# Kernel optimization log

Measured on AMD Instinct MI355X. Metric: run time of the kernel, lower is better.

## Reference

```python
import jax, jax.numpy as jnp
import numpy as np

B, N = 8192, 20
D_IN = 256       # input_dim / neigh_input_dim
G_IN = 128       # geto_dims_in
H = 201 * 3      # hidden_dim, model_size='small'
D_OUT = 256      # output_dim


def _glorot(key, shape):
    lim = np.sqrt(6.0 / (shape[0] + shape[1]))
    return jax.random.uniform(key, shape, jnp.float32, -lim, lim)


def setup_inputs() -> dict:
    key = jax.random.key(0)
    ks = jax.random.split(key, 16)
    return {
        "self_vecs": jax.random.normal(ks[0], (B, D_IN), jnp.float32),
        "neigh_vecs": jax.random.normal(ks[1], (B, N, D_IN), jnp.float32),
        "self_geto": jax.random.normal(ks[2], (B, G_IN), jnp.float32),
        "neigh_geto": jax.random.normal(ks[3], (B, N, G_IN), jnp.float32),
        # feat MLP (relu)
        "W_feat": _glorot(ks[4], (D_IN, H)),
        "b_feat": jnp.zeros((H,), jnp.float32),
        # geto MLP (relu)
        "W_geto": _glorot(ks[5], (G_IN, H)),
        "b_geto": jnp.zeros((H,), jnp.float32),
        # geto-concat MLP (softmax act)
        "W_concat": _glorot(ks[6], (G_IN, H)),
        "b_concat": jnp.zeros((H,), jnp.float32),
        # combine weights
        "self_feat_w": _glorot(ks[7], (D_IN, D_OUT)),
        "self_geto_w": _glorot(ks[8], (G_IN, D_OUT)),
        "combined_geto": _glorot(ks[9], (H, 2 * D_OUT)),
        "neigh_feat_w": _glorot(ks[10], (H, D_OUT)),
        "neigh_geto_w": _glorot(ks[11], (H, D_OUT)),
    }


def reference(self_vecs, neigh_vecs, self_geto, neigh_geto,
              W_feat, b_feat, W_geto, b_geto, W_concat, b_concat,
              self_feat_w, self_geto_w, combined_geto,
              neigh_feat_w, neigh_geto_w):
    # --- geto-concat branch: Dense(softmax) over self+neighbor geto, mean pool ---
    geto_cat = jnp.concatenate([neigh_geto, self_geto[:, None, :]], axis=1)  # [B,N+1,G]
    geto_hidden = jax.nn.softmax(
        jnp.einsum('bng,gh->bnh', geto_cat, W_concat) + b_concat, axis=-1)   # [B,N+1,H]
    geto_pool = jnp.mean(geto_hidden, axis=1)                                # [B,H]
    from_geto_embedding = geto_pool @ combined_geto                          # [B,2*out]

    # --- neighbor feature branch: Dense(relu), mean pool, project ---
    neigh_h = jax.nn.relu(jnp.einsum('bnd,dh->bnh', neigh_vecs, W_feat) + b_feat)
    from_neigh_feat = jnp.mean(neigh_h, axis=1) @ neigh_feat_w               # [B,out]
    from_self_feat = self_vecs @ self_feat_w                                 # [B,out]
    from_feat_embedding = jnp.concatenate([from_self_feat, from_neigh_feat], axis=1)

    weighted_embedding = from_geto_embedding * from_feat_embedding           # [B,2*out]

    # --- neighbor geto branch: Dense(relu), mean pool, project ---
    neigh_g_h = jax.nn.relu(jnp.einsum('bng,gh->bnh', neigh_geto, W_geto) + b_geto)
    from_neigh_geto = jnp.mean(neigh_g_h, axis=1) @ neigh_geto_w             # [B,out]
    from_self_geto = self_geto @ self_geto_w                                 # [B,out]

    node_output = jax.nn.relu(weighted_embedding)          # concat=False, bias=False
    geto_output = jax.nn.relu(from_self_geto + from_neigh_geto)
    return node_output, geto_output
```

## Files before the change

kernel.cpp:

```cpp
#include <hip/hip_runtime.h>
#include <hip/hip_bf16.h>

#define B_SZ   8192
#define NNEI   20
#define DIN    256
#define GIN    128
#define HID    603
#define DOUT   256
#define NT_TOTAL 38

using short8  = __attribute__((ext_vector_type(8))) short;
using float4v = __attribute__((ext_vector_type(4))) float;

__device__ __forceinline__ unsigned short f2bf_bits(float x) {
  unsigned int u = __builtin_bit_cast(unsigned int, x);
  unsigned int r = 0x7fffu + ((u >> 16) & 1u);
  u += r;
  return (unsigned short)(u >> 16);
}
__device__ __forceinline__ float bf2f(unsigned short h) {
  unsigned int u = ((unsigned int)h) << 16;
  return __builtin_bit_cast(float, u);
}

template <int K>
__global__ __launch_bounds__(256) void pack_w_kernel(
    const float* __restrict__ W, short* __restrict__ Wh, short* __restrict__ Wl) {
  constexpr int TOT = NT_TOTAL * (K / 8) * 16 * 8;
  int p = blockIdx.x * 256 + threadIdx.x;
  if (p >= TOT) return;
  int j  = p & 7;
  int cc = (p >> 3) & 15;
  int kb = (p >> 7) % (K / 8);
  int nt = p / (128 * (K / 8));
  int k   = kb * 8 + j;
  int col = nt * 16 + cc;
  float v = (col < HID) ? W[(size_t)k * HID + col] : 0.f;
  unsigned short h = f2bf_bits(v);
  float lo = v - bf2f(h);
  Wh[p] = (short)h;
  Wl[p] = (short)f2bf_bits(lo);
}

template <int ROWS, int K, int ACT>
__global__ __launch_bounds__(256) void pooled_mfma_kernel(
    const float* __restrict__ A_neigh,
    const float* __restrict__ A_self,
    const short* __restrict__ Wh,
    const short* __restrict__ Wl,
    const float* __restrict__ bias,
    float* __restrict__ P) {
  __shared__ short AsH[32][K];
  __shared__ short AsL[32][K];
  __shared__ float redA[4][32];
  __shared__ float redB[4][32];

  const int b    = blockIdx.x;
  const int tid  = threadIdx.x;
  const int w    = tid >> 6;
  const int lane = tid & 63;
  const int g    = lane >> 4;
  const int c    = lane & 15;

  constexpr int NEIGH_ROWS = (ACT == 1) ? (ROWS - 1) : ROWS;
  constexpr int NV4 = 32 * K / 4 / 256;
#pragma unroll
  for (int i = 0; i < NV4; i++) {
    int idx = tid + i * 256;
    int row = idx / (K / 4);
    int kq  = idx % (K / 4);
    float4 v = make_float4(0.f, 0.f, 0.f, 0.f);
    if (row < ROWS) {
      if (ACT == 1 && row == ROWS - 1)
        v = ((const float4*)A_self)[(size_t)b * (K / 4) + kq];
      else
        v = ((const float4*)A_neigh)[((size_t)b * NEIGH_ROWS + row) * (K / 4) + kq];
    }
    float x[4] = {v.x, v.y, v.z, v.w};
    ushort4 hh, ll;
    unsigned short* hp = &hh.x;
    unsigned short* lp = &ll.x;
#pragma unroll
    for (int q = 0; q < 4; q++) {
      unsigned short h = f2bf_bits(x[q]);
      hp[q] = h;
      lp[q] = f2bf_bits(x[q] - bf2f(h));
    }
    *(ushort4*)&AsH[row][kq * 4] = hh;
    *(ushort4*)&AsL[row][kq * 4] = ll;
  }
  __syncthreads();

  constexpr int NTW = 10;
  const int nt0 = w * NTW;
  float4v acc[2][NTW];
#pragma unroll
  for (int mt = 0; mt < 2; mt++)
#pragma unroll
    for (int t = 0; t < NTW; t++) acc[mt][t] = (float4v){0.f, 0.f, 0.f, 0.f};

  for (int k0 = 0; k0 < K; k0 += 32) {
    short8 ah[2], al[2];
#pragma unroll
    for (int mt = 0; mt < 2; mt++) {
      ah[mt] = *(const short8*)&AsH[mt * 16 + c][k0 + 8 * g];
      al[mt] = *(const short8*)&AsL[mt * 16 + c][k0 + 8 * g];
    }
#pragma unroll
    for (int t = 0; t < NTW; t++) {
      int nt = nt0 + t;
      if (nt < NT_TOTAL) {
        const size_t base = (((size_t)nt * (K / 8) + (k0 / 8 + g)) * 16 + c) * 8;
        short8 wh = *(const short8*)&Wh[base];
        short8 wl = *(const short8*)&Wl[base];
#pragma unroll
        for (int mt = 0; mt < 2; mt++) {
          acc[mt][t] = __builtin_amdgcn_mfma_f32_16x16x32_bf16(ah[mt], wh, acc[mt][t], 0, 0, 0);
          acc[mt][t] = __builtin_amdgcn_mfma_f32_16x16x32_bf16(al[mt], wh, acc[mt][t], 0, 0, 0);
          acc[mt][t] = __builtin_amdgcn_mfma_f32_16x16x32_bf16(ah[mt], wl, acc[mt][t], 0, 0, 0);
        }
      }
    }
  }

  float bc[NTW];
#pragma unroll
  for (int t = 0; t < NTW; t++) {
    int nt = nt0 + t;
    int col = nt * 16 + c;
    bc[t] = (nt < NT_TOTAL && col < HID) ? bias[col] : 0.f;
  }

  if constexpr (ACT == 0) {
    float pool[NTW];
#pragma unroll
    for (int t = 0; t < NTW; t++) {
      float s = 0.f;
#pragma unroll
      for (int mt = 0; mt < 2; mt++)
#pragma unroll
        for (int q = 0; q < 4; q++) {
          int row = mt * 16 + g * 4 + q;
          if (row < ROWS) s += fmaxf(acc[mt][t][q] + bc[t], 0.f);
        }
      pool[t] = s;
    }
#pragma unroll
    for (int t = 0; t < NTW; t++) {
      pool[t] += __shfl_xor(pool[t], 16, 64);
      pool[t] += __shfl_xor(pool[t], 32, 64);
    }
    if (g == 0) {
#pragma unroll
      for (int t = 0; t < NTW; t++) {
        int nt = nt0 + t;
        int col = nt * 16 + c;
        if (nt < NT_TOTAL && col < HID)
          P[(size_t)b * HID + col] = pool[t] * (1.f / (float)ROWS);
      }
    }
  } else {
#pragma unroll
    for (int t = 0; t < NTW; t++) {
      int nt = nt0 + t;
      int col = nt * 16 + c;
      bool cv = (nt < NT_TOTAL) && (col < HID);
#pragma unroll
      for (int mt = 0; mt < 2; mt++)
#pragma unroll
        for (int q = 0; q < 4; q++)
          acc[mt][t][q] = cv ? (acc[mt][t][q] + bc[t]) : -1e30f;
    }
    float rm[2][4];
#pragma unroll
    for (int mt = 0; mt < 2; mt++)
#pragma unroll
      for (int q = 0; q < 4; q++) {
        float m = -1e30f;
#pragma unroll
        for (int t = 0; t < NTW; t++) m = fmaxf(m, acc[mt][t][q]);
        rm[mt][q] = m;
      }
#pragma unroll
    for (int mt = 0; mt < 2; mt++)
#pragma unroll
      for (int q = 0; q < 4; q++) {
#pragma unroll
        for (int msk = 1; msk <= 8; msk <<= 1)
          rm[mt][q] = fmaxf(rm[mt][q], __shfl_xor(rm[mt][q], msk, 64));
      }
    if (c == 0) {
#pragma unroll
      for (int mt = 0; mt < 2; mt++)
#pragma unroll
        for (int q = 0; q < 4; q++) redA[w][mt * 16 + g * 4 + q] = rm[mt][q];
    }
    __syncthreads();
#pragma unroll
    for (int mt = 0; mt < 2; mt++)
#pragma unroll
      for (int q = 0; q < 4; q++) {
        int row = mt * 16 + g * 4 + q;
        rm[mt][q] = fmaxf(fmaxf(redA[0][row], redA[1][row]),
                          fmaxf(redA[2][row], redA[3][row]));
      }
    float rs[2][4] = {{0.f, 0.f, 0.f, 0.f}, {0.f, 0.f, 0.f, 0.f}};
#pragma unroll
    for (int t = 0; t < NTW; t++)
#pragma unroll
      for (int mt = 0; mt < 2; mt++)
#pragma unroll
        for (int q = 0; q < 4; q++) {
          float e = __expf(acc[mt][t][q] - rm[mt][q]);
          acc[mt][t][q] = e;
          rs[mt][q] += e;
        }
#pragma unroll
    for (int mt = 0; mt < 2; mt++)
#pragma unroll
      for (int q = 0; q < 4; q++) {
#pragma unroll
        for (int msk = 1; msk <= 8; msk <<= 1)
          rs[mt][q] += __shfl_xor(rs[mt][q], msk, 64);
      }
    if (c == 0) {
#pragma unroll
      for (int mt = 0; mt < 2; mt++)
#pragma unroll
        for (int q = 0; q < 4; q++) redB[w][mt * 16 + g * 4 + q] = rs[mt][q];
    }
    __syncthreads();
    float rinv[2][4];
#pragma unroll
    for (int mt = 0; mt < 2; mt++)
#pragma unroll
      for (int q = 0; q < 4; q++) {
        int row = mt * 16 + g * 4 + q;
        rinv[mt][q] = 1.f / (redB[0][row] + redB[1][row] + redB[2][row] + redB[3][row]);
      }
    float pool[NTW];
#pragma unroll
    for (int t = 0; t < NTW; t++) {
      float s = 0.f;
#pragma unroll
      for (int mt = 0; mt < 2; mt++)
#pragma unroll
        for (int q = 0; q < 4; q++) {
          int row = mt * 16 + g * 4 + q;
          if (row < ROWS) s += acc[mt][t][q] * rinv[mt][q];
        }
      pool[t] = s;
    }
#pragma unroll
    for (int t = 0; t < NTW; t++) {
      pool[t] += __shfl_xor(pool[t], 16, 64);
      pool[t] += __shfl_xor(pool[t], 32, 64);
    }
    if (g == 0) {
#pragma unroll
      for (int t = 0; t < NTW; t++) {
        int nt = nt0 + t;
        int col = nt * 16 + c;
        if (nt < NT_TOTAL && col < HID)
          P[(size_t)b * HID + col] = pool[t] * (1.f / (float)ROWS);
      }
    }
  }
}

template <int COMBINE>
__global__ __launch_bounds__(256) void dual_gemm_kernel(
    const float* __restrict__ A1, int K1,
    const float* __restrict__ W1, int ldw1, int w1off,
    const float* __restrict__ A2, int K2,
    const float* __restrict__ W2, int ldw2, int w2off,
    float* __restrict__ out, int ldo, int ooff) {
  __shared__ float Ats[32][68];
  __shared__ float Ws[32][64];

  const int tid = threadIdx.x;
  const int tx = tid & 15;
  const int ty = tid >> 4;
  const int row0 = blockIdx.x * 64;
  const int col0 = blockIdx.y * 64;

  float acc1[4][4];
  float acc2[4][4];
#pragma unroll
  for (int i = 0; i < 4; i++)
#pragma unroll
    for (int j = 0; j < 4; j++) {
      acc1[i][j] = 0.f;
      acc2[i][j] = 0.f;
    }

  auto gemm_phase = [&](const float* __restrict__ A, int K,
                        const float* __restrict__ W, int ldw, int woff,
                        float (&acc)[4][4]) {
    for (int k0 = 0; k0 < K; k0 += 32) {
      __syncthreads();
#pragma unroll
      for (int ii = 0; ii < 8; ii++) {
        int i = tid + ii * 256;
        int r = i >> 5;
        int k = i & 31;
        float v = (k0 + k < K) ? A[(size_t)(row0 + r) * K + k0 + k] : 0.f;
        Ats[k][r] = v;
      }
#pragma unroll
      for (int ii = 0; ii < 8; ii++) {
        int i = tid + ii * 256;
        int k = i >> 6;
        int cj = i & 63;
        float v = (k0 + k < K) ? W[(size_t)(k0 + k) * ldw + woff + col0 + cj] : 0.f;
        Ws[k][cj] = v;
      }
      __syncthreads();
#pragma unroll
      for (int kk = 0; kk < 32; kk++) {
        float4 a = *(const float4*)&Ats[kk][ty * 4];
        float4 w = *(const float4*)&Ws[kk][tx * 4];
        float av[4] = {a.x, a.y, a.z, a.w};
        float wv[4] = {w.x, w.y, w.z, w.w};
#pragma unroll
        for (int i2 = 0; i2 < 4; i2++)
#pragma unroll
          for (int j2 = 0; j2 < 4; j2++)
            acc[i2][j2] = fmaf(av[i2], wv[j2], acc[i2][j2]);
      }
    }
  };

  gemm_phase(A1, K1, W1, ldw1, w1off, acc1);
  gemm_phase(A2, K2, W2, ldw2, w2off, acc2);

#pragma unroll
  for (int i2 = 0; i2 < 4; i2++) {
    int r = row0 + ty * 4 + i2;
    float4 o;
    float vals[4];
#pragma unroll
    for (int j2 = 0; j2 < 4; j2++) {
      float v = (COMBINE == 0) ? acc1[i2][j2] * acc2[i2][j2]
                               : acc1[i2][j2] + acc2[i2][j2];
      vals[j2] = fmaxf(v, 0.f);
    }
    o.x = vals[0]; o.y = vals[1]; o.z = vals[2]; o.w = vals[3];
    *(float4*)&out[(size_t)r * ldo + ooff + col0 + tx * 4] = o;
  }
}

extern "C" void kernel_launch(void* const* d_in, const int* in_sizes, int n_in,
                              void* d_out, int out_size, void* d_ws,
                              size_t ws_size, hipStream_t stream) {
  const float* self_vecs     = (const float*)d_in[0];
  const float* neigh_vecs    = (const float*)d_in[1];
  const float* self_geto     = (const float*)d_in[2];
  const float* neigh_geto    = (const float*)d_in[3];
  const float* W_feat        = (const float*)d_in[4];
  const float* b_feat        = (const float*)d_in[5];
  const float* W_geto        = (const float*)d_in[6];
  const float* b_geto        = (const float*)d_in[7];
  const float* W_concat      = (const float*)d_in[8];
  const float* b_concat      = (const float*)d_in[9];
  const float* self_feat_w   = (const float*)d_in[10];
  const float* self_geto_w   = (const float*)d_in[11];
  const float* combined_geto = (const float*)d_in[12];
  const float* neigh_feat_w  = (const float*)d_in[13];
  const float* neigh_geto_w  = (const float*)d_in[14];
  float* out = (float*)d_out;

  float* P_concat = (float*)d_ws;
  float* P_feat   = P_concat + (size_t)B_SZ * HID;
  float* P_geto   = P_feat + (size_t)B_SZ * HID;

  constexpr int WPF = NT_TOTAL * (DIN / 8) * 16 * 8;
  constexpr int WPG = NT_TOTAL * (GIN / 8) * 16 * 8;
  short* Wh_feat = (short*)(P_geto + (size_t)B_SZ * HID);
  short* Wl_feat = Wh_feat + WPF;
  short* Wh_geto = Wl_feat + WPF;
  short* Wl_geto = Wh_geto + WPG;
  short* Wh_cc   = Wl_geto + WPG;
  short* Wl_cc   = Wh_cc + WPG;

  pack_w_kernel<DIN><<<(WPF + 255) / 256, 256, 0, stream>>>(W_feat, Wh_feat, Wl_feat);
  pack_w_kernel<GIN><<<(WPG + 255) / 256, 256, 0, stream>>>(W_geto, Wh_geto, Wl_geto);
  pack_w_kernel<GIN><<<(WPG + 255) / 256, 256, 0, stream>>>(W_concat, Wh_cc, Wl_cc);

  pooled_mfma_kernel<21, GIN, 1><<<B_SZ, 256, 0, stream>>>(
      neigh_geto, self_geto, Wh_cc, Wl_cc, b_concat, P_concat);
  pooled_mfma_kernel<20, DIN, 0><<<B_SZ, 256, 0, stream>>>(
      neigh_vecs, nullptr, Wh_feat, Wl_feat, b_feat, P_feat);
  pooled_mfma_kernel<20, GIN, 0><<<B_SZ, 256, 0, stream>>>(
      neigh_geto, nullptr, Wh_geto, Wl_geto, b_geto, P_geto);

  dim3 g2(B_SZ / 64, DOUT / 64);
  dual_gemm_kernel<0><<<g2, 256, 0, stream>>>(
      P_concat, HID, combined_geto, 2 * DOUT, 0,
      self_vecs, DIN, self_feat_w, DOUT, 0,
      out, 2 * DOUT, 0);
  dual_gemm_kernel<0><<<g2, 256, 0, stream>>>(
      P_concat, HID, combined_geto, 2 * DOUT, DOUT,
      P_feat, HID, neigh_feat_w, DOUT, 0,
      out, 2 * DOUT, DOUT);
  dual_gemm_kernel<1><<<g2, 256, 0, stream>>>(
      self_geto, GIN, self_geto_w, DOUT, 0,
      P_geto, HID, neigh_geto_w, DOUT, 0,
      out + (size_t)B_SZ * 2 * DOUT, DOUT, 0);
}
```

Baseline: 1.542 ms.

## Pack several batch rows per block and drop bf16 split for ReLU stages

Replaces the one-batch-per-block pooled MFMA kernels with kernels that pack multiple batch items (8 for ReLU branches, 3 for softmax) into the MFMA M dimension, pooling via LDS atomics. Rows are loaded straight from global into registers instead of through LDS, wasting fewer padded rows and reusing each weight fragment across more rows. The ReLU branches now use single bf16 (truncated) precision instead of the 3-MFMA hi/lo split, which cuts MFMA work but lowers accuracy. The softmax branch keeps the split, with truncation in place of rounding for the hi part.

```diff
diff --git a/kernel.cpp b/kernel.cpp
--- a/kernel.cpp
+++ b/kernel.cpp
@@ -2,7 +2,6 @@
 #include <hip/hip_bf16.h>
 
 #define B_SZ   8192
-#define NNEI   20
 #define DIN    256
 #define GIN    128
 #define HID    603
@@ -12,6 +11,8 @@
 using short8  = __attribute__((ext_vector_type(8))) short;
 using float4v = __attribute__((ext_vector_type(4))) float;
 
+#define MFMA16 __builtin_amdgcn_mfma_f32_16x16x32_bf16
+
 __device__ __forceinline__ unsigned short f2bf_bits(float x) {
   unsigned int u = __builtin_bit_cast(unsigned int, x);
   unsigned int r = 0x7fffu + ((u >> 16) & 1u);
@@ -21,6 +22,11 @@
 __device__ __forceinline__ float bf2f(unsigned short h) {
   unsigned int u = ((unsigned int)h) << 16;
   return __builtin_bit_cast(float, u);
+}
+__device__ __forceinline__ unsigned int pack_bf16_trunc(float f0, float f1) {
+  return __builtin_amdgcn_perm(__builtin_bit_cast(unsigned int, f1),
+                               __builtin_bit_cast(unsigned int, f0),
+                               0x07060302u);
 }
 
 template <int K>
@@ -42,229 +48,305 @@
   Wl[p] = (short)f2bf_bits(lo);
 }
 
-template <int ROWS, int K, int ACT>
-__global__ __launch_bounds__(256) void pooled_mfma_kernel(
-    const float* __restrict__ A_neigh,
-    const float* __restrict__ A_self,
+template <int ROWS, int K, int NB, int MT>
+__global__ __launch_bounds__(256, 3) void stage1_relu_kernel(
+    const float* __restrict__ A,
     const short* __restrict__ Wh,
-    const short* __restrict__ Wl,
     const float* __restrict__ bias,
     float* __restrict__ P) {
-  __shared__ short AsH[32][K];
-  __shared__ short AsL[32][K];
-  __shared__ float redA[4][32];
-  __shared__ float redB[4][32];
-
-  const int b    = blockIdx.x;
+  constexpr int KS  = K / 32;
+  constexpr int MTP = MT / 2;
+  __shared__ float pool[NB][609];
+
   const int tid  = threadIdx.x;
   const int w    = tid >> 6;
   const int lane = tid & 63;
   const int g    = lane >> 4;
   const int c    = lane & 15;
-
-  constexpr int NEIGH_ROWS = (ACT == 1) ? (ROWS - 1) : ROWS;
-  constexpr int NV4 = 32 * K / 4 / 256;
-#pragma unroll
-  for (int i = 0; i < NV4; i++) {
-    int idx = tid + i * 256;
-    int row = idx / (K / 4);
-    int kq  = idx % (K / 4);
-    float4 v = make_float4(0.f, 0.f, 0.f, 0.f);
-    if (row < ROWS) {
-      if (ACT == 1 && row == ROWS - 1)
-        v = ((const float4*)A_self)[(size_t)b * (K / 4) + kq];
-      else
-        v = ((const float4*)A_neigh)[((size_t)b * NEIGH_ROWS + row) * (K / 4) + kq];
-    }
-    float x[4] = {v.x, v.y, v.z, v.w};
-    ushort4 hh, ll;
-    unsigned short* hp = &hh.x;
-    unsigned short* lp = &ll.x;
-#pragma unroll
-    for (int q = 0; q < 4; q++) {
-      unsigned short h = f2bf_bits(x[q]);
-      hp[q] = h;
-      lp[q] = f2bf_bits(x[q] - bf2f(h));
-    }
-    *(ushort4*)&AsH[row][kq * 4] = hh;
-    *(ushort4*)&AsL[row][kq * 4] = ll;
-  }
+  const int bbase = blockIdx.x * NB;
+
+  for (int i = tid; i < NB * 609; i += 256) (&pool[0][0])[i] = 0.f;
   __syncthreads();
 
+  const int nt0 = w * 10;
+  const int ntw = min(10, NT_TOTAL - nt0);
+
+  for (int mtp = 0; mtp < MTP; mtp++) {
+    short8 ah[2][KS];
+    int b0i[2], b1i[2], spl[2];
+#pragma unroll
+    for (int m2 = 0; m2 < 2; m2++) {
+      int row = (mtp * 2 + m2) * 16 + c;
+      int bl  = row / ROWS;
+      int rr  = row - bl * ROWS;
+      const float* src = A + ((size_t)(bbase + bl) * ROWS + rr) * K + g * 8;
+#pragma unroll
+      for (int ks = 0; ks < KS; ks++) {
+        float4 f0 = *(const float4*)(src + ks * 32);
+        float4 f1 = *(const float4*)(src + ks * 32 + 4);
+        union { unsigned int u[4]; short8 s; } r;
+        r.u[0] = pack_bf16_trunc(f0.x, f0.y);
+        r.u[1] = pack_bf16_trunc(f0.z, f0.w);
+        r.u[2] = pack_bf16_trunc(f1.x, f1.y);
+        r.u[3] = pack_bf16_trunc(f1.z, f1.w);
+        ah[m2][ks] = r.s;
+      }
+      int r0 = (mtp * 2 + m2) * 16 + g * 4;
+      b0i[m2] = r0 / ROWS;
+      b1i[m2] = (r0 + 3) / ROWS;
+      spl[m2] = b1i[m2] * ROWS - r0;
+    }
+
+    for (int t = 0; t < ntw; t++) {
+      int nt = nt0 + t;
+      float4v acc[2];
+#pragma unroll
+      for (int m2 = 0; m2 < 2; m2++) acc[m2] = (float4v){0.f, 0.f, 0.f, 0.f};
+      const short* wp = Wh + (((size_t)nt * (K / 8) + g) * 16 + c) * 8;
+#pragma unroll
+      for (int ks = 0; ks < KS; ks++) {
+        short8 wf = *(const short8*)(wp + (size_t)ks * 512);
+        acc[0] = MFMA16(ah[0][ks], wf, acc[0], 0, 0, 0);
+        acc[1] = MFMA16(ah[1][ks], wf, acc[1], 0, 0, 0);
+      }
+      int col = nt * 16 + c;
+      if (col < HID) {
+        float bc = bias[col];
+#pragma unroll
+        for (int m2 = 0; m2 < 2; m2++) {
+          float v[4];
+#pragma unroll
+          for (int q = 0; q < 4; q++) v[q] = fmaxf(acc[m2][q] + bc, 0.f);
+          if (b0i[m2] == b1i[m2]) {
+            atomicAdd(&pool[b0i[m2]][col], v[0] + v[1] + v[2] + v[3]);
+          } else {
+            float sA = 0.f, sB = 0.f;
+#pragma unroll
+            for (int q = 0; q < 4; q++) {
+              if (q < spl[m2]) sA += v[q]; else sB += v[q];
+            }
+            atomicAdd(&pool[b0i[m2]][col], sA);
+            atomicAdd(&pool[b1i[m2]][col], sB);
+          }
+        }
+      }
+    }
+  }
+  __syncthreads();
+  for (int i = tid; i < NB * HID; i += 256) {
+    int bl = i / HID, col = i - bl * HID;
+    P[((size_t)(bbase + bl)) * HID + col] = pool[bl][col] * (1.f / (float)ROWS);
+  }
+}
+
+template <int ROWS, int K, int NB, int MT>
+__global__ __launch_bounds__(256, 2) void stage1_softmax_kernel(
+    const float* __restrict__ An,
+    const float* __restrict__ Asf,
+    const short* __restrict__ Wh, const short* __restrict__ Wl,
+    const float* __restrict__ bias,
+    float* __restrict__ P) {
+  constexpr int KS  = K / 32;
+  constexpr int MTP = MT / 2;
   constexpr int NTW = 10;
-  const int nt0 = w * NTW;
-  float4v acc[2][NTW];
-#pragma unroll
-  for (int mt = 0; mt < 2; mt++)
-#pragma unroll
-    for (int t = 0; t < NTW; t++) acc[mt][t] = (float4v){0.f, 0.f, 0.f, 0.f};
-
-  for (int k0 = 0; k0 < K; k0 += 32) {
-    short8 ah[2], al[2];
-#pragma unroll
-    for (int mt = 0; mt < 2; mt++) {
-      ah[mt] = *(const short8*)&AsH[mt * 16 + c][k0 + 8 * g];
-      al[mt] = *(const short8*)&AsL[mt * 16 + c][k0 + 8 * g];
-    }
+  __shared__ float pool[NB][609];
+  __shared__ float redm[4][32];
+  __shared__ float reds[4][32];
+
+  const int tid  = threadIdx.x;
+  const int w    = tid >> 6;
+  const int lane = tid & 63;
+  const int g    = lane >> 4;
+  const int c    = lane & 15;
+  const int bbase = blockIdx.x * NB;
+
+  for (int i = tid; i < NB * 609; i += 256) (&pool[0][0])[i] = 0.f;
+  __syncthreads();
+
+  const int nt0 = w * 10;
+  const int ntw = min(10, NT_TOTAL - nt0);
+
+  float bias_t[NTW];
+#pragma unroll
+  for (int t = 0; t < NTW; t++) {
+    int nt = nt0 + t, col = nt * 16 + c;
+    bias_t[t] = (nt < NT_TOTAL && col < HID) ? bias[col] : 0.f;
+  }
+
+  for (int mtp = 0; mtp < MTP; mtp++) {
+    short8 ah[2][KS], al[2][KS];
+    int b0i[2], b1i[2], spl[2];
+#pragma unroll
+    for (int m2 = 0; m2 < 2; m2++) {
+      int row = (mtp * 2 + m2) * 16 + c;
+      int bl  = row / ROWS;
+      int rr  = row - bl * ROWS;
+      int gb  = bbase + bl;
+      bool valid = (bl < NB) && (gb < B_SZ);
+      const float* src = (rr == ROWS - 1)
+          ? (Asf + (size_t)gb * K + g * 8)
+          : (An + ((size_t)gb * (ROWS - 1) + rr) * K + g * 8);
+#pragma unroll
+      for (int ks = 0; ks < KS; ks++) {
+        float4 f0 = make_float4(0.f, 0.f, 0.f, 0.f);
+        float4 f1 = make_float4(0.f, 0.f, 0.f, 0.f);
+        if (valid) {
+          f0 = *(const float4*)(src + ks * 32);
+          f1 = *(const float4*)(src + ks * 32 + 4);
+        }
+        float fv[8] = {f0.x, f0.y, f0.z, f0.w, f1.x, f1.y, f1.z, f1.w};
+        float hf[8], lf[8];
+#pragma unroll
+        for (int j = 0; j < 8; j++) {
+          unsigned int hu = __builtin_bit_cast(unsigned int, fv[j]) & 0xFFFF0000u;
+          hf[j] = __builtin_bit_cast(float, hu);
+          lf[j] = fv[j] - hf[j];
+        }
+        union { unsigned int u[4]; short8 s; } rh, rl;
+#pragma unroll
+        for (int p = 0; p < 4; p++) {
+          rh.u[p] = pack_bf16_trunc(hf[2 * p], hf[2 * p + 1]);
+          rl.u[p] = pack_bf16_trunc(lf[2 * p], lf[2 * p + 1]);
+        }
+        ah[m2][ks] = rh.s;
+        al[m2][ks] = rl.s;
+      }
+      int r0 = (mtp * 2 + m2) * 16 + g * 4;
+      b0i[m2] = r0 / ROWS;
+      b1i[m2] = (r0 + 3) / ROWS;
+      spl[m2] = b1i[m2] * ROWS - r0;
+    }
+
+    float4v acc[2][NTW];
+#pragma unroll
+    for (int m2 = 0; m2 < 2; m2++)
+#pragma unroll
+      for (int t = 0; t < NTW; t++) acc[m2][t] = (float4v){0.f, 0.f, 0.f, 0.f};
+
 #pragma unroll
     for (int t = 0; t < NTW; t++) {
-      int nt = nt0 + t;
-      if (nt < NT_TOTAL) {
-        const size_t base = (((size_t)nt * (K / 8) + (k0 / 8 + g)) * 16 + c) * 8;
-        short8 wh = *(const short8*)&Wh[base];
-        short8 wl = *(const short8*)&Wl[base];
-#pragma unroll
-        for (int mt = 0; mt < 2; mt++) {
-          acc[mt][t] = __builtin_amdgcn_mfma_f32_16x16x32_bf16(ah[mt], wh, acc[mt][t], 0, 0, 0);
-          acc[mt][t] = __builtin_amdgcn_mfma_f32_16x16x32_bf16(al[mt], wh, acc[mt][t], 0, 0, 0);
-          acc[mt][t] = __builtin_amdgcn_mfma_f32_16x16x32_bf16(ah[mt], wl, acc[mt][t], 0, 0, 0);
-        }
-      }
-    }
-  }
-
-  float bc[NTW];
-#pragma unroll
-  for (int t = 0; t < NTW; t++) {
-    int nt = nt0 + t;
-    int col = nt * 16 + c;
-    bc[t] = (nt < NT_TOTAL && col < HID) ? bias[col] : 0.f;
-  }
-
-  if constexpr (ACT == 0) {
-    float pool[NTW];
-#pragma unroll
-    for (int t = 0; t < NTW; t++) {
-      float s = 0.f;
-#pragma unroll
-      for (int mt = 0; mt < 2; mt++)
-#pragma unroll
-        for (int q = 0; q < 4; q++) {
-          int row = mt * 16 + g * 4 + q;
-          if (row < ROWS) s += fmaxf(acc[mt][t][q] + bc[t], 0.f);
-        }
-      pool[t] = s;
-    }
-#pragma unroll
-    for (int t = 0; t < NTW; t++) {
-      pool[t] += __shfl_xor(pool[t], 16, 64);
-      pool[t] += __shfl_xor(pool[t], 32, 64);
-    }
-    if (g == 0) {
+      if (t < ntw) {
+        int nt = nt0 + t;
+        const short* wph = Wh + (((size_t)nt * (K / 8) + g) * 16 + c) * 8;
+        const short* wpl = Wl + (((size_t)nt * (K / 8) + g) * 16 + c) * 8;
+#pragma unroll
+        for (int ks = 0; ks < KS; ks++) {
+          short8 wh = *(const short8*)(wph + (size_t)ks * 512);
+          short8 wl = *(const short8*)(wpl + (size_t)ks * 512);
+#pragma unroll
+          for (int m2 = 0; m2 < 2; m2++) {
+            acc[m2][t] = MFMA16(ah[m2][ks], wh, acc[m2][t], 0, 0, 0);
+            acc[m2][t] = MFMA16(al[m2][ks], wh, acc[m2][t], 0, 0, 0);
+            acc[m2][t] = MFMA16(ah[m2][ks], wl, acc[m2][t], 0, 0, 0);
+          }
+        }
+      }
+    }
+
+#pragma unroll
+    for (int m2 = 0; m2 < 2; m2++)
 #pragma unroll
       for (int t = 0; t < NTW; t++) {
-        int nt = nt0 + t;
-        int col = nt * 16 + c;
-        if (nt < NT_TOTAL && col < HID)
-          P[(size_t)b * HID + col] = pool[t] * (1.f / (float)ROWS);
-      }
-    }
-  } else {
-#pragma unroll
-    for (int t = 0; t < NTW; t++) {
-      int nt = nt0 + t;
-      int col = nt * 16 + c;
-      bool cv = (nt < NT_TOTAL) && (col < HID);
-#pragma unroll
-      for (int mt = 0; mt < 2; mt++)
-#pragma unroll
-        for (int q = 0; q < 4; q++)
-          acc[mt][t][q] = cv ? (acc[mt][t][q] + bc[t]) : -1e30f;
-    }
+        if (t < ntw) {
+          int col = (nt0 + t) * 16 + c;
+          bool cv = col < HID;
+#pragma unroll
+          for (int q = 0; q < 4; q++)
+            acc[m2][t][q] = cv ? (acc[m2][t][q] + bias_t[t]) : -1e30f;
+        }
+      }
     float rm[2][4];
 #pragma unroll
-    for (int mt = 0; mt < 2; mt++)
+    for (int m2 = 0; m2 < 2; m2++)
 #pragma unroll
       for (int q = 0; q < 4; q++) {
         float m = -1e30f;
 #pragma unroll
-        for (int t = 0; t < NTW; t++) m = fmaxf(m, acc[mt][t][q]);
-        rm[mt][q] = m;
-      }
-#pragma unroll
-    for (int mt = 0; mt < 2; mt++)
+        for (int t = 0; t < NTW; t++)
+          if (t < ntw) m = fmaxf(m, acc[m2][t][q]);
+#pragma unroll
+        for (int msk = 1; msk <= 8; msk <<= 1)
+          m = fmaxf(m, __shfl_xor(m, msk, 64));
+        rm[m2][q] = m;
+      }
+    if (c == 0) {
+#pragma unroll
+      for (int m2 = 0; m2 < 2; m2++)
+#pragma unroll
+        for (int q = 0; q < 4; q++) redm[w][m2 * 16 + g * 4 + q] = rm[m2][q];
+    }
+    __syncthreads();
+#pragma unroll
+    for (int m2 = 0; m2 < 2; m2++)
 #pragma unroll
       for (int q = 0; q < 4; q++) {
+        int idx = m2 * 16 + g * 4 + q;
+        rm[m2][q] = fmaxf(fmaxf(redm[0][idx], redm[1][idx]),
+                          fmaxf(redm[2][idx], redm[3][idx]));
+      }
+    float rs[2][4];
+#pragma unroll
+    for (int m2 = 0; m2 < 2; m2++)
+#pragma unroll
+      for (int q = 0; q < 4; q++) {
+        float s = 0.f;
+#pragma unroll
+        for (int t = 0; t < NTW; t++) {
+          if (t < ntw) {
+            float e = __expf(acc[m2][t][q] - rm[m2][q]);
+            acc[m2][t][q] = e;
+            s += e;
+          }
+        }
 #pragma unroll
         for (int msk = 1; msk <= 8; msk <<= 1)
-          rm[mt][q] = fmaxf(rm[mt][q], __shfl_xor(rm[mt][q], msk, 64));
+          s += __shfl_xor(s, msk, 64);
+        rs[m2][q] = s;
       }
     if (c == 0) {
 #pragma unroll
-      for (int mt = 0; mt < 2; mt++)
-#pragma unroll
-        for (int q = 0; q < 4; q++) redA[w][mt * 16 + g * 4 + q] = rm[mt][q];
-    }
-    __syncthreads();
-#pragma unroll
-    for (int mt = 0; mt < 2; mt++)
-#pragma unroll
-      for (int q = 0; q < 4; q++) {
-        int row = mt * 16 + g * 4 + q;
-        rm[mt][q] = fmaxf(fmaxf(redA[0][row], redA[1][row]),
-                          fmaxf(redA[2][row], redA[3][row]));
-      }
-    float rs[2][4] = {{0.f, 0.f, 0.f, 0.f}, {0.f, 0.f, 0.f, 0.f}};
-#pragma unroll
-    for (int t = 0; t < NTW; t++)
-#pragma unroll
-      for (int mt = 0; mt < 2; mt++)
-#pragma unroll
-        for (int q = 0; q < 4; q++) {
-          float e = __expf(acc[mt][t][q] - rm[mt][q]);
-          acc[mt][t][q] = e;
-          rs[mt][q] += e;
-        }
-#pragma unroll
-    for (int mt = 0; mt < 2; mt++)
-#pragma unroll
-      for (int q = 0; q < 4; q++) {
-#pragma unroll
-        for (int msk = 1; msk <= 8; msk <<= 1)
-          rs[mt][q] += __shfl_xor(rs[mt][q], msk, 64);
-      }
-    if (c == 0) {
-#pragma unroll
-      for (int mt = 0; mt < 2; mt++)
-#pragma unroll
-        for (int q = 0; q < 4; q++) redB[w][mt * 16 + g * 4 + q] = rs[mt][q];
+      for (int m2 = 0; m2 < 2; m2++)
+#pragma unroll
+        for (int q = 0; q < 4; q++) reds[w][m2 * 16 + g * 4 + q] = rs[m2][q];
     }
     __syncthreads();
     float rinv[2][4];
 #pragma unroll
-    for (int mt = 0; mt < 2; mt++)
+    for (int m2 = 0; m2 < 2; m2++)
 #pragma unroll
       for (int q = 0; q < 4; q++) {
-        int row = mt * 16 + g * 4 + q;
-        rinv[mt][q] = 1.f / (redB[0][row] + redB[1][row] + redB[2][row] + redB[3][row]);
-      }
-    float pool[NTW];
+        int idx = m2 * 16 + g * 4 + q;
+        rinv[m2][q] = 1.f / (reds[0][idx] + reds[1][idx] + reds[2][idx] + reds[3][idx]);
+      }
 #pragma unroll
     for (int t = 0; t < NTW; t++) {
-      float s = 0.f;
-#pragma unroll
-      for (int mt = 0; mt < 2; mt++)
-#pragma unroll
-        for (int q = 0; q < 4; q++) {
-          int row = mt * 16 + g * 4 + q;
-          if (row < ROWS) s += acc[mt][t][q] * rinv[mt][q];
-        }
-      pool[t] = s;
-    }
-#pragma unroll
-    for (int t = 0; t < NTW; t++) {
-      pool[t] += __shfl_xor(pool[t], 16, 64);
-      pool[t] += __shfl_xor(pool[t], 32, 64);
-    }
-    if (g == 0) {
-#pragma unroll
-      for (int t = 0; t < NTW; t++) {
-        int nt = nt0 + t;
-        int col = nt * 16 + c;
-        if (nt < NT_TOTAL && col < HID)
-          P[(size_t)b * HID + col] = pool[t] * (1.f / (float)ROWS);
-      }
-    }
+      if (t < ntw) {
+        int col = (nt0 + t) * 16 + c;
+        if (col < HID) {
+#pragma unroll
+          for (int m2 = 0; m2 < 2; m2++) {
+            float sA = 0.f, sB = 0.f;
+#pragma unroll
+            for (int q = 0; q < 4; q++) {
+              float e = acc[m2][t][q] * rinv[m2][q];
+              if (q < spl[m2]) sA += e; else sB += e;
+            }
+            bool vb0 = (b0i[m2] < NB) && (bbase + b0i[m2] < B_SZ);
+            bool vb1 = (b1i[m2] < NB) && (bbase + b1i[m2] < B_SZ) &&
+                       (b1i[m2] != b0i[m2]);
+            if (vb0) atomicAdd(&pool[b0i[m2]][col], sA);
+            if (vb1) atomicAdd(&pool[b1i[m2]][col], sB);
+          }
+        }
+      }
+    }
+  }
+  __syncthreads();
+  for (int i = tid; i < NB * HID; i += 256) {
+    int bl = i / HID, col = i - bl * HID;
+    int gb = bbase + bl;
+    if (gb < B_SZ)
+      P[(size_t)gb * HID + col] = pool[bl][col] * (1.f / (float)ROWS);
   }
 }
 
@@ -387,12 +469,12 @@
   pack_w_kernel<GIN><<<(WPG + 255) / 256, 256, 0, stream>>>(W_geto, Wh_geto, Wl_geto);
   pack_w_kernel<GIN><<<(WPG + 255) / 256, 256, 0, stream>>>(W_concat, Wh_cc, Wl_cc);
 
-  pooled_mfma_kernel<21, GIN, 1><<<B_SZ, 256, 0, stream>>>(
+  stage1_softmax_kernel<21, GIN, 3, 4><<<(B_SZ + 2) / 3, 256, 0, stream>>>(
       neigh_geto, self_geto, Wh_cc, Wl_cc, b_concat, P_concat);
-  pooled_mfma_kernel<20, DIN, 0><<<B_SZ, 256, 0, stream>>>(
-      neigh_vecs, nullptr, Wh_feat, Wl_feat, b_feat, P_feat);
-  pooled_mfma_kernel<20, GIN, 0><<<B_SZ, 256, 0, stream>>>(
-      neigh_geto, nullptr, Wh_geto, Wl_geto, b_geto, P_geto);
+  stage1_relu_kernel<20, DIN, 8, 10><<<B_SZ / 8, 256, 0, stream>>>(
+      neigh_vecs, Wh_feat, b_feat, P_feat);
+  stage1_relu_kernel<20, GIN, 8, 10><<<B_SZ / 8, 256, 0, stream>>>(
+      neigh_geto, Wh_geto, b_geto, P_geto);
 
   dim3 g2(B_SZ / 64, DOUT / 64);
   dual_gemm_kernel<0><<<g2, 256, 0, stream>>>(
```

Measured after the change: 1.282 ms. 1.2x faster.
